# Kernel optimization log

Hardware: AMD Instinct MI355X
Metric: run time of the kernel (lower is better)

The kernel has to match this reference:

```python
import jax, jax.numpy as jnp
import numpy as np

B = 131072
IN = 128
H = 128

def setup_inputs() -> dict:
    key = jax.random.key(0)
    ks = jax.random.split(key, 12)
    # kaiming-normal-ish init for weights (std ~ sqrt(2/fan_out))
    std_w = (2.0 / H) ** 0.5
    inp = {
        'x': jax.random.normal(ks[0], (B, IN), dtype=jnp.float32),
        'h_prev': jax.random.normal(ks[1], (B, H), dtype=jnp.float32),
        'c_prev': jax.random.normal(ks[2], (B, H), dtype=jnp.float32),
        'Wi': jax.random.normal(ks[3], (IN, H), dtype=jnp.float32) * std_w,
        'Ui': jax.random.normal(ks[4], (H, H), dtype=jnp.float32) * std_w,
        'bi': jnp.ones((H,), dtype=jnp.float32),
        'Wf': jax.random.normal(ks[5], (IN, H), dtype=jnp.float32) * std_w,
        'Uf': jax.random.normal(ks[6], (H, H), dtype=jnp.float32) * std_w,
        'bf': jnp.ones((H,), dtype=jnp.float32),
        'Wg': jax.random.normal(ks[7], (IN, H), dtype=jnp.float32) * std_w,
        'Ug': jax.random.normal(ks[8], (H, H), dtype=jnp.float32) * std_w,
        'bg': jnp.ones((H,), dtype=jnp.float32),
        'Wo': jax.random.normal(ks[9], (IN, H), dtype=jnp.float32) * std_w,
        'Uo': jax.random.normal(ks[10], (H, H), dtype=jnp.float32) * std_w,
        'bo': jnp.ones((H,), dtype=jnp.float32),
    }
    return inp

def reference(x, h_prev, c_prev, Wi, Ui, bi, Wf, Uf, bf, Wg, Ug, bg, Wo, Uo, bo):
    # Faithful per-gate math (i, f, o sigmoid gates; g tanh candidate)
    ig = jax.nn.sigmoid(x @ Wi + h_prev @ Ui + bi)
    fg = jax.nn.sigmoid(x @ Wf + h_prev @ Uf + bf)
    og = jax.nn.sigmoid(x @ Wo + h_prev @ Uo + bo)
    cc = jnp.tanh(x @ Wg + h_prev @ Ug + bg)
    c = fg * c_prev + ig * cc
    h = og * jnp.tanh(c)
    return (h, c)
```

## Files before the change

kernel.cpp:

```cpp
#include <hip/hip_runtime.h>


#define B_ROWS 131072
#define HDIM 128
#define KDIM 256
#define BM 64

typedef __attribute__((ext_vector_type(4))) float f32x4;
typedef __attribute__((ext_vector_type(8))) short s16x8;

__device__ inline unsigned short f2bf(float f) {
    unsigned int u = __float_as_uint(f);
    u += 0x7fffu + ((u >> 16) & 1u);
    return (unsigned short)(u >> 16);
}

__device__ inline float frcp(float x) { return __builtin_amdgcn_rcpf(x); }
__device__ inline float fsigmoid(float x) { return frcp(1.0f + __expf(-x)); }
__device__ inline float ftanh(float x) { return 1.0f - 2.0f * frcp(__expf(2.0f * x) + 1.0f); }

__global__ void prep_weights(const float* __restrict__ Wi, const float* __restrict__ Ui,
                             const float* __restrict__ Wf, const float* __restrict__ Uf,
                             const float* __restrict__ Wg, const float* __restrict__ Ug,
                             const float* __restrict__ Wo, const float* __restrict__ Uo,
                             unsigned short* __restrict__ Bp) {
    int idx = blockIdx.x * 256 + threadIdx.x;
    int e   = idx & 7;
    int q   = (idx >> 3) & 3;
    int t16 = (idx >> 5) & 15;
    int ni  = (idx >> 9) & 3;
    int kc  = (idx >> 11) & 7;
    int w   = idx >> 14;
    int j = w * 16 + t16;
    int k = kc * 32 + q * 8 + e;
    const float* Wp = ni == 0 ? Wi : ni == 1 ? Wf : ni == 2 ? Wg : Wo;
    const float* Up = ni == 0 ? Ui : ni == 1 ? Uf : ni == 2 ? Ug : Uo;
    float v = (k < 128) ? Wp[k * HDIM + j] : Up[(k - 128) * HDIM + j];
    Bp[idx] = f2bf(v);
}

__global__ __launch_bounds__(512, 4) void lstm_main(
    const float* __restrict__ x, const float* __restrict__ h_prev,
    const float* __restrict__ c_prev,
    const unsigned short* __restrict__ Bp,
    const float* __restrict__ bi, const float* __restrict__ bf_,
    const float* __restrict__ bg, const float* __restrict__ bo,
    float* __restrict__ out)
{
    __shared__ unsigned short As[4 * 8 * 512];

    const int tid = threadIdx.x;
    const int m0 = blockIdx.x * BM;

    #pragma unroll
    for (int it = 0; it < 8; ++it) {
        int fi = it * 512 + tid;
        int r  = fi >> 6;
        int c4 = fi & 63;
        int k0 = c4 * 4;
        const float* src = (k0 < 128) ? (x + (size_t)(m0 + r) * HDIM + k0)
                                      : (h_prev + (size_t)(m0 + r) * HDIM + (k0 - 128));
        float4 v = *(const float4*)src;
        ushort4 p;
        p.x = f2bf(v.x); p.y = f2bf(v.y); p.z = f2bf(v.z); p.w = f2bf(v.w);
        int mi = r >> 4, t16r = r & 15;
        int kc = k0 >> 5, qq = (k0 >> 3) & 3, e0 = k0 & 7;
        *(ushort4*)&As[((mi * 8 + kc) * 16 + t16r) * 32 + qq * 8 + e0] = p;
    }
    __syncthreads();

    const int wave = tid >> 6;
    const int lane = tid & 63;
    const int t16 = lane & 15;
    const int q = lane >> 4;
    const int lane_off = t16 * 32 + q * 8;

    f32x4 acc[4][4];
    const f32x4 zero = {0.0f, 0.0f, 0.0f, 0.0f};
    #pragma unroll
    for (int mi = 0; mi < 4; ++mi)
        #pragma unroll
        for (int ni = 0; ni < 4; ++ni)
            acc[mi][ni] = zero;

    const unsigned short* bbase = Bp + (size_t)(wave * 8) * 2048 + lane_off;

    #pragma unroll
    for (int kc = 0; kc < 8; ++kc) {
        s16x8 a[4], b[4];
        #pragma unroll
        for (int ni = 0; ni < 4; ++ni)
            b[ni] = *(const s16x8*)(bbase + kc * 2048 + ni * 512);
        #pragma unroll
        for (int mi = 0; mi < 4; ++mi)
            a[mi] = *(const s16x8*)&As[(mi * 8 + kc) * 512 + lane_off];
        #pragma unroll
        for (int mi = 0; mi < 4; ++mi)
            #pragma unroll
            for (int ni = 0; ni < 4; ++ni)
                acc[mi][ni] = __builtin_amdgcn_mfma_f32_16x16x32_bf16(a[mi], b[ni], acc[mi][ni], 0, 0, 0);
    }

    const int j = wave * 16 + t16;
    const float vbi = bi[j], vbf = bf_[j], vbg = bg[j], vbo = bo[j];
    float* hout = out;
    float* cout = out + (size_t)B_ROWS * HDIM;

    float cp[4][4];
    #pragma unroll
    for (int mi = 0; mi < 4; ++mi)
        #pragma unroll
        for (int r = 0; r < 4; ++r)
            cp[mi][r] = c_prev[(size_t)(m0 + mi * 16 + q * 4 + r) * HDIM + j];

    #pragma unroll
    for (int mi = 0; mi < 4; ++mi) {
        #pragma unroll
        for (int r = 0; r < 4; ++r) {
            int row = m0 + mi * 16 + q * 4 + r;
            size_t off = (size_t)row * HDIM + j;
            float ig = fsigmoid(acc[mi][0][r] + vbi);
            float fg = fsigmoid(acc[mi][1][r] + vbf);
            float cc = ftanh(acc[mi][2][r] + vbg);
            float og = fsigmoid(acc[mi][3][r] + vbo);
            float c = fg * cp[mi][r] + ig * cc;
            float h = og * ftanh(c);
            hout[off] = h;
            cout[off] = c;
        }
    }
}

extern "C" void kernel_launch(void* const* d_in, const int* in_sizes, int n_in,
                              void* d_out, int out_size, void* d_ws, size_t ws_size,
                              hipStream_t stream) {
    const float* x      = (const float*)d_in[0];
    const float* h_prev = (const float*)d_in[1];
    const float* c_prev = (const float*)d_in[2];
    const float* Wi = (const float*)d_in[3];
    const float* Ui = (const float*)d_in[4];
    const float* bi = (const float*)d_in[5];
    const float* Wf = (const float*)d_in[6];
    const float* Uf = (const float*)d_in[7];
    const float* bf = (const float*)d_in[8];
    const float* Wg = (const float*)d_in[9];
    const float* Ug = (const float*)d_in[10];
    const float* bg = (const float*)d_in[11];
    const float* Wo = (const float*)d_in[12];
    const float* Uo = (const float*)d_in[13];
    const float* bo = (const float*)d_in[14];

    unsigned short* Bp = (unsigned short*)d_ws;

    prep_weights<<<512, 256, 0, stream>>>(Wi, Ui, Wf, Uf, Wg, Ug, Wo, Uo, Bp);
    lstm_main<<<B_ROWS / BM, 512, 0, stream>>>(x, h_prev, c_prev, Bp, bi, bf, bg, bo, (float*)d_out);
}
```

Baseline: 347.7 us.

## Stage LSTM c_prev loads and h/c outputs through LDS for coalesced float4 access

The c_prev tile is now read with row-contiguous float4 loads, before the GEMM, into a padded LDS buffer. The gate epilogue writes h and c into padded LDS tiles, which are then copied out with coalesced float4 stores. This replaces the old scattered per-row 4-byte global loads and stores, where each wave touched only 64-byte segments. LDS use per block roughly doubles, so fewer blocks fit per CU, and the change adds two more block-wide barriers.

New measurement: 328.8 us. 5.4% less time.

```diff
diff --git a/kernel.cpp b/kernel.cpp
--- a/kernel.cpp
+++ b/kernel.cpp
@@ -5,6 +5,7 @@
 #define HDIM 128
 #define KDIM 256
 #define BM 64
+#define LDT 132
 
 typedef __attribute__((ext_vector_type(4))) float f32x4;
 typedef __attribute__((ext_vector_type(8))) short s16x8;
@@ -47,10 +48,21 @@
     const float* __restrict__ bg, const float* __restrict__ bo,
     float* __restrict__ out)
 {
-    __shared__ unsigned short As[4 * 8 * 512];
+    __shared__ float smem[2 * BM * LDT];
+    float* hbuf = smem;
+    float* cbuf = smem + BM * LDT;
+    unsigned short* As = (unsigned short*)smem;
 
     const int tid = threadIdx.x;
     const int m0 = blockIdx.x * BM;
+
+    float4 cpv[4];
+    #pragma unroll
+    for (int it = 0; it < 4; ++it) {
+        int f = it * 512 + tid;
+        int r = f >> 5, c4 = f & 31;
+        cpv[it] = *(const float4*)(c_prev + (size_t)(m0 + r) * HDIM + c4 * 4);
+    }
 
     #pragma unroll
     for (int it = 0; it < 8; ++it) {
@@ -66,6 +78,13 @@
         int mi = r >> 4, t16r = r & 15;
         int kc = k0 >> 5, qq = (k0 >> 3) & 3, e0 = k0 & 7;
         *(ushort4*)&As[((mi * 8 + kc) * 16 + t16r) * 32 + qq * 8 + e0] = p;
+    }
+
+    #pragma unroll
+    for (int it = 0; it < 4; ++it) {
+        int f = it * 512 + tid;
+        int r = f >> 5, c4 = f & 31;
+        *(float4*)&cbuf[r * LDT + c4 * 4] = cpv[it];
     }
     __syncthreads();
 
@@ -100,34 +119,38 @@
             for (int ni = 0; ni < 4; ++ni)
                 acc[mi][ni] = __builtin_amdgcn_mfma_f32_16x16x32_bf16(a[mi], b[ni], acc[mi][ni], 0, 0, 0);
     }
+    __syncthreads();
 
     const int j = wave * 16 + t16;
     const float vbi = bi[j], vbf = bf_[j], vbg = bg[j], vbo = bo[j];
-    float* hout = out;
-    float* cout = out + (size_t)B_ROWS * HDIM;
-
-    float cp[4][4];
-    #pragma unroll
-    for (int mi = 0; mi < 4; ++mi)
-        #pragma unroll
-        for (int r = 0; r < 4; ++r)
-            cp[mi][r] = c_prev[(size_t)(m0 + mi * 16 + q * 4 + r) * HDIM + j];
 
     #pragma unroll
     for (int mi = 0; mi < 4; ++mi) {
         #pragma unroll
         for (int r = 0; r < 4; ++r) {
-            int row = m0 + mi * 16 + q * 4 + r;
-            size_t off = (size_t)row * HDIM + j;
+            int rt = mi * 16 + q * 4 + r;
+            float cp = cbuf[rt * LDT + j];
             float ig = fsigmoid(acc[mi][0][r] + vbi);
             float fg = fsigmoid(acc[mi][1][r] + vbf);
             float cc = ftanh(acc[mi][2][r] + vbg);
             float og = fsigmoid(acc[mi][3][r] + vbo);
-            float c = fg * cp[mi][r] + ig * cc;
+            float c = fg * cp + ig * cc;
             float h = og * ftanh(c);
-            hout[off] = h;
-            cout[off] = c;
+            hbuf[rt * LDT + j] = h;
+            cbuf[rt * LDT + j] = c;
         }
+    }
+    __syncthreads();
+
+    float* hout = out;
+    float* cout = out + (size_t)B_ROWS * HDIM;
+    #pragma unroll
+    for (int it = 0; it < 4; ++it) {
+        int f = it * 512 + tid;
+        int r = f >> 5, c4 = f & 31;
+        size_t goff = (size_t)(m0 + r) * HDIM + c4 * 4;
+        *(float4*)(hout + goff) = *(const float4*)&hbuf[r * LDT + c4 * 4];
+        *(float4*)(cout + goff) = *(const float4*)&cbuf[r * LDT + c4 * 4];
     }
 }
 
```
